# Optimization experiments

Measured on AMD Instinct MI355X. Metric: run time of the kernel, lower is better.

## Reference

```python
import jax, jax.numpy as jnp
import numpy as np

KNN = 5
MAX_STEPS = 100
LAM = 1.0  # bound_lambda


def setup_inputs() -> dict:
    key = jax.random.key(0)
    k1, k2 = jax.random.split(key)
    # probabilities in (0,1): softmax-like scores
    scores_raw = jax.random.uniform(k1, (1, 8192, 8, 8), dtype=jnp.float32)
    feats = jax.random.normal(k2, (1, 8192, 256, 1, 1), dtype=jnp.float32)
    return {"scores_raw": scores_raw, "feats": feats}


def knn_affinity(X, knn):
    # X: (N, D) L2-normalized features. Same math as torch.norm(x_i - x_j):
    # ||xi-xj|| = sqrt(|xi|^2 + |xj|^2 - 2 xi.xj), avoids the O(N^2 D) broadcast.
    N = X.shape[0]
    sq = jnp.sum(X * X, axis=-1)                                  # (N,)
    dist2 = sq[:, None] + sq[None, :] - 2.0 * (X @ X.T)           # (N, N)
    dist = jnp.sqrt(jnp.maximum(dist2, 0.0))
    n_neighbors = min(knn + 1, N)
    _, idx = jax.lax.top_k(-dist, n_neighbors)                    # smallest distances
    idx = idx[:, 1:]                                              # drop self
    W = jnp.zeros((N, N), X.dtype).at[jnp.arange(N)[:, None], idx].set(1.0)
    return W


def reference(scores_raw, feats):
    _, _, H, W = scores_raw.shape
    unary = -jnp.log(scores_raw.reshape(-1, H * W) + 1e-10)       # (N, K)
    f = feats.reshape(feats.shape[0], feats.shape[1], -1)[0]       # (N, D), flatten(-3).squeeze(0)
    nrm = jnp.linalg.norm(f, axis=-1, keepdims=True)
    f = f / jnp.maximum(nrm, 1e-12)                                # F.normalize(p=2)
    kernel = knn_affinity(f, KNN)                                  # (N, N)

    Y0 = jax.nn.softmax(-unary, axis=-1)

    def cond(state):
        i, Y, oldE, conv = state
        return (i < MAX_STEPS) & (~conv)

    def body(state):
        i, Y, oldE, _ = state
        pairwise = LAM * (kernel @ Y)                              # (N, K)
        Ynew = jax.nn.softmax(-unary + pairwise, axis=-1)
        # entropy_energy (note: lambda multiplies pairwise again, as in source)
        E = jnp.sum(unary * Ynew - LAM * pairwise * Ynew
                    + Ynew * jnp.log(jnp.clip(Ynew, 1e-20)))
        conv = (i > 1) & (jnp.abs(E - oldE) <= 1e-8 * jnp.abs(oldE))
        return (i + 1, Ynew, E, conv)

    init = (jnp.int32(0), Y0, jnp.float32(jnp.inf), jnp.bool_(False))
    _, Y, _, _ = jax.lax.while_loop(cond, body, init)
    return Y
```

## Files before the change

kernel.cpp:

```cpp
#include <hip/hip_runtime.h>
#include <math.h>

#define NROWS 8192
#define DIM   256
#define NCLS  64
#define KNN   5
#define NCAND 8
#define NSPLIT 4
#define MAXSTEPS 100
#define PBLK 256

struct GS {
  double Eold;
  double Epart[PBLK];
  int pad0[30];
  int gcnt[16 * 32];
  int root; int pad1[31];
  int gen;  int pad2[31];
  int flag; int pad3[31];
};

typedef __attribute__((ext_vector_type(8))) short bf16x8;
typedef __attribute__((ext_vector_type(4))) float f32x4;

typedef __attribute__((address_space(1))) unsigned int glb_u32_t;
typedef __attribute__((address_space(3))) unsigned int lds_u32_t;
__device__ __forceinline__ void async_cp16(const uint4* g, uint4* l) {
  __builtin_amdgcn_global_load_lds((const glb_u32_t*)(const unsigned int*)g,
                                   (lds_u32_t*)(unsigned int*)l, 16, 0, 0);
}

__device__ __forceinline__ float aloadf(const float* p) {
  return __hip_atomic_load(p, __ATOMIC_RELAXED, __HIP_MEMORY_SCOPE_AGENT);
}
__device__ __forceinline__ void astoref(float* p, float v) {
  __hip_atomic_store(p, v, __ATOMIC_RELAXED, __HIP_MEMORY_SCOPE_AGENT);
}
__device__ __forceinline__ double aloadd(const double* p) {
  return __hip_atomic_load(p, __ATOMIC_RELAXED, __HIP_MEMORY_SCOPE_AGENT);
}
__device__ __forceinline__ void astored(double* p, double v) {
  __hip_atomic_store(p, v, __ATOMIC_RELAXED, __HIP_MEMORY_SCOPE_AGENT);
}
__device__ __forceinline__ int aloadi(const int* p) {
  return __hip_atomic_load(p, __ATOMIC_RELAXED, __HIP_MEMORY_SCOPE_AGENT);
}
__device__ __forceinline__ void astorei(int* p, int v) {
  __hip_atomic_store(p, v, __ATOMIC_RELAXED, __HIP_MEMORY_SCOPE_AGENT);
}
__device__ __forceinline__ int afetchadd(int* p) {
  return __hip_atomic_fetch_add(p, 1, __ATOMIC_RELAXED, __HIP_MEMORY_SCOPE_AGENT);
}

__device__ __forceinline__ float wave_sum64(float v) {
#pragma unroll
  for (int m = 32; m >= 1; m >>= 1) v += __shfl_xor(v, m, 64);
  return v;
}
__device__ __forceinline__ double wave_sum64d(double v) {
#pragma unroll
  for (int m = 32; m >= 1; m >>= 1) v += __shfl_xor(v, m, 64);
  return v;
}

__device__ __forceinline__ unsigned short f2bf(float x) {
  unsigned u = __float_as_uint(x);
  u += 0x7FFFu + ((u >> 16) & 1u);
  return (unsigned short)(u >> 16);
}

__global__ void k_normalize(const float* __restrict__ feats, uint2* __restrict__ fb2,
                            float* __restrict__ f, double* __restrict__ sqd) {
  int row  = blockIdx.x * 4 + (threadIdx.x >> 6);
  int lane = threadIdx.x & 63;
  float4 v = ((const float4*)(feats + (size_t)row * DIM))[lane];
  double ss = (double)v.x * v.x + (double)v.y * v.y + (double)v.z * v.z + (double)v.w * v.w;
  ss = wave_sum64d(ss);
  float nr = fmaxf((float)sqrt(ss), 1e-12f);
  float4 o;
  o.x = v.x / nr; o.y = v.y / nr; o.z = v.z / nr; o.w = v.w / nr;
  ((float4*)(f + (size_t)row * DIM))[lane] = o;
  double s2 = (double)o.x * o.x + (double)o.y * o.y + (double)o.z * o.z + (double)o.w * o.w;
  s2 = wave_sum64d(s2);
  if (lane == 0) sqd[row] = s2;
  uint2 w2;
  w2.x = (unsigned)f2bf(o.x) | ((unsigned)f2bf(o.y) << 16);
  w2.y = (unsigned)f2bf(o.z) | ((unsigned)f2bf(o.w) << 16);
  int T = row >> 6, rl = row & 63, g = lane >> 1, h = lane & 1;
  fb2[((size_t)T * 2048 + rl * 32 + (g ^ (rl & 31))) * 2 + h] = w2;
}

#define JSPAN (NROWS / NSPLIT)
#define GTILES (JSPAN / 64)

__launch_bounds__(256, 2)
__global__ void k_gram(const uint4* __restrict__ fb, int* __restrict__ candp) {
  __shared__ uint4 Bsh4[2][2048];
  __shared__ float Csh[4096];

  const int t  = threadIdx.x;
  const int ib = blockIdx.x >> 2;
  const int js = blockIdx.x & 3;
  const int i0 = ib * 64;
  const int jbase = js * JSPAN;
  const int w = t >> 6, lane = t & 63;

  {
    const uint4* At = fb + (size_t)ib * 2048;
    const uint4* Bt = fb + (size_t)(js * 32) * 2048;
#pragma unroll
    for (int p = 0; p < 8; ++p) {
      int c = w * 8 + p;
      async_cp16(At + c * 64 + lane, &Bsh4[1][c * 64]);
      async_cp16(Bt + c * 64 + lane, &Bsh4[0][c * 64]);
    }
  }
  const int ihalf = w >> 1, jhalf = w & 1;
  const int m15 = lane & 15, quad = lane >> 4;

  __syncthreads();

  bf16x8 areg[2][8];
#pragma unroll
  for (int s = 0; s < 2; ++s) {
    int ra = ihalf * 32 + s * 16 + m15;
#pragma unroll
    for (int kc = 0; kc < 8; ++kc)
      areg[s][kc] = ((const bf16x8*)Bsh4[1])[ra * 32 + ((kc * 4 + quad) ^ (ra & 31))];
  }
  __syncthreads();

  unsigned mk[NCAND];
#pragma unroll
  for (int k = 0; k < NCAND; ++k) mk[k] = 0u;
  float thr = -1e30f;

  const int trow = lane >> 1;
  const int thalf = lane & 1;
  float* Csw = Csh + w * 1024;

  for (int jt = 0; jt < GTILES; ++jt) {
    const int cbuf = jt & 1;
    if (jt > 0) __syncthreads();
    if (jt + 1 < GTILES) {
      const uint4* Bt = fb + (size_t)(js * 32 + jt + 1) * 2048;
#pragma unroll
      for (int p = 0; p < 8; ++p) {
        int c = w * 8 + p;
        async_cp16(Bt + c * 64 + lane, &Bsh4[1 - cbuf][c * 64]);
      }
    }

    f32x4 acc[2][2];
#pragma unroll
    for (int si = 0; si < 2; ++si)
#pragma unroll
      for (int sj = 0; sj < 2; ++sj) acc[si][sj] = (f32x4)(0.f);

#pragma unroll
    for (int kc = 0; kc < 8; ++kc) {
      bf16x8 bv[2];
#pragma unroll
      for (int s = 0; s < 2; ++s) {
        int rb = jhalf * 32 + s * 16 + m15;
        bv[s] = ((const bf16x8*)Bsh4[cbuf])[rb * 32 + ((kc * 4 + quad) ^ (rb & 31))];
      }
      acc[0][0] = __builtin_amdgcn_mfma_f32_16x16x32_bf16(areg[0][kc], bv[0], acc[0][0], 0, 0, 0);
      acc[0][1] = __builtin_amdgcn_mfma_f32_16x16x32_bf16(areg[0][kc], bv[1], acc[0][1], 0, 0, 0);
      acc[1][0] = __builtin_amdgcn_mfma_f32_16x16x32_bf16(areg[1][kc], bv[0], acc[1][0], 0, 0, 0);
      acc[1][1] = __builtin_amdgcn_mfma_f32_16x16x32_bf16(areg[1][kc], bv[1], acc[1][1], 0, 0, 0);
    }

#pragma unroll
    for (int si = 0; si < 2; ++si)
#pragma unroll
      for (int sj = 0; sj < 2; ++sj) {
        int lr0 = si * 16 + quad * 4;
        int key = quad * 2;
        int lc = sj * 16 + m15;
        int gc = lc >> 2;
        int base = lr0 * 32 + ((gc ^ key) << 2) + (lc & 3);
#pragma unroll
        for (int r = 0; r < 4; ++r)
          Csw[base + r * 32] = acc[si][sj][r];
      }

    {
      int cb0 = jt * 64 + jhalf * 32;
      int skey = (trow >> 1) & 6;
#pragma unroll
      for (int p = 0; p < 4; ++p) {
        int gc = thalf * 4 + p;
        float4 v = *(const float4*)&Csw[trow * 32 + ((gc ^ skey) << 2)];
        float g4 = fmaxf(fmaxf(v.x, v.y), fmaxf(v.z, v.w));
        if (g4 > thr) {
          int cbase = cb0 + gc * 4;
          float vv[4] = {v.x, v.y, v.z, v.w};
#pragma unroll
          for (int e = 0; e < 4; ++e) {
            unsigned ub = __float_as_uint(vv[e]);
            unsigned key = ((ub ^ (unsigned)(((int)ub >> 31) | 0x80000000)) & ~2047u)
                           | (unsigned)(cbase + e);
            if (key > mk[NCAND - 1]) {
              mk[NCAND - 1] = key;
#pragma unroll
              for (int q = NCAND - 1; q >= 1; --q)
                if (mk[q] > mk[q - 1]) { unsigned tm = mk[q]; mk[q] = mk[q - 1]; mk[q - 1] = tm; }
            }
          }
          unsigned kb = mk[NCAND - 1] & ~2047u;
          if (kb) {
            unsigned xm = 0x80000000u | ~(unsigned)((int)kb >> 31);
            thr = __uint_as_float(kb ^ xm);
          }
        }
      }
    }
  }

  __syncthreads();
  unsigned* mergeK = (unsigned*)Csh;
  {
    int grow = ihalf * 32 + trow;
    int q = jhalf * 2 + thalf;
#pragma unroll
    for (int k = 0; k < NCAND; ++k) mergeK[grow * 33 + q * 8 + k] = mk[k];
  }
  __syncthreads();
  if (t < 64) {
    unsigned fk[NCAND];
#pragma unroll
    for (int k = 0; k < NCAND; ++k) fk[k] = 0u;
    for (int s = 0; s < 32; ++s) {
      unsigned kk = mergeK[t * 33 + s];
      if (kk > fk[NCAND - 1]) {
        fk[NCAND - 1] = kk;
#pragma unroll
        for (int q = NCAND - 1; q >= 1; --q)
          if (fk[q] > fk[q - 1]) { unsigned tm = fk[q]; fk[q] = fk[q - 1]; fk[q - 1] = tm; }
      }
    }
#pragma unroll
    for (int k = 0; k < NCAND; ++k)
      candp[(size_t)js * (NROWS * NCAND) + (size_t)(i0 + t) * NCAND + k] =
          jbase + (int)(fk[k] & 2047u);
  }
}

__global__ void k_refine(const float* __restrict__ f, const double* __restrict__ sqd,
                         const int* __restrict__ candp, int* __restrict__ nbr) {
  const int row = blockIdx.x * 4 + (threadIdx.x >> 6);
  const int t = threadIdx.x & 63;
  const int c = t >> 1;
  const int seg = t & 1;
  const int split = c >> 3, slot = c & 7;
  int j = candp[(size_t)split * (NROWS * NCAND) + (size_t)row * NCAND + slot];
  const float4* fi4 = (const float4*)(f + (size_t)row * DIM) + seg * 32;
  const float4* fj4 = (const float4*)(f + (size_t)j * DIM) + seg * 32;
  double dot = 0.0;
#pragma unroll 8
  for (int d4 = 0; d4 < 32; ++d4) {
    float4 a = fi4[d4], b = fj4[d4];
    dot = fma((double)a.x, (double)b.x, dot);
    dot = fma((double)a.y, (double)b.y, dot);
    dot = fma((double)a.z, (double)b.z, dot);
    dot = fma((double)a.w, (double)b.w, dot);
  }
  dot += __shfl_xor(dot, 1, 64);
  double key = sqd[j] - 2.0 * dot;
  bool valid = (seg == 0) && (j != row);
  for (int s = 0; s < KNN; ++s) {
    double v = valid ? key : (double)INFINITY;
    int vj = valid ? j : 0x7fffffff;
#pragma unroll
    for (int m = 1; m < 64; m <<= 1) {
      double ov = __shfl_xor(v, m, 64);
      int oj = __shfl_xor(vj, m, 64);
      if (ov < v || (ov == v && oj < vj)) { v = ov; vj = oj; }
    }
    if (valid && vj == j) valid = false;
    if (t == 0) nbr[(size_t)row * 8 + s] = vj;
  }
}

__global__ void k_solve(const float* __restrict__ scores,
                        const int* __restrict__ nbr,
                        float* __restrict__ Ya, float* __restrict__ Yb,
                        float* __restrict__ out, GS* __restrict__ gs) {
  const int b = blockIdx.x;
  const int w = threadIdx.x >> 6, lane = threadIdx.x & 63;
  const int row0 = b * 32 + w * 4;
  const int grp = (b & 15) * 32;
  __shared__ int nbl[32][5];
  __shared__ double sE[8];
  __shared__ int sflag;

  if (threadIdx.x < 160)
    nbl[threadIdx.x / 5][threadIdx.x % 5] =
        nbr[(size_t)(b * 32 + threadIdx.x / 5) * 8 + (threadIdx.x % 5)];

  float u[4], y[4];
#pragma unroll
  for (int r = 0; r < 4; ++r)
    u[r] = -logf(scores[(size_t)(row0 + r) * NCLS + lane] + 1e-10f);
#pragma unroll
  for (int r = 0; r < 4; ++r) {
    float e = expf(-u[r]);
    float sum = wave_sum64(e);
    y[r] = e / sum;
    astoref(&Ya[(size_t)(row0 + r) * NCLS + lane], y[r]);
  }
  __syncthreads();

  int nboff[4][KNN];
#pragma unroll
  for (int r = 0; r < 4; ++r)
#pragma unroll
    for (int k = 0; k < KNN; ++k)
      nboff[r][k] = nbl[w * 4 + r][k] * NCLS + lane;

  int mygen = 1;
  if (threadIdx.x == 0) {
    __builtin_amdgcn_fence(__ATOMIC_RELEASE, "workgroup");
    int old = afetchadd(&gs->gcnt[grp]);
    if (old == 15) {
      int r = afetchadd(&gs->root);
      if (r == 15) {
#pragma unroll
        for (int m = 0; m < 16; ++m) astorei(&gs->gcnt[m * 32], 0);
        astorei(&gs->root, 0);
        __builtin_amdgcn_fence(__ATOMIC_RELEASE, "workgroup");
        astorei(&gs->gen, mygen);
      }
    }
    while (aloadi(&gs->gen) < mygen) __builtin_amdgcn_s_sleep(1);
  }
  __syncthreads();
  ++mygen;

  for (int iter = 0; iter < MAXSTEPS; ++iter) {
    const float* __restrict__ Yin = (iter & 1) ? Yb : Ya;
    float* __restrict__ Yout = (iter & 1) ? Ya : Yb;
    double ew = 0.0;
#pragma unroll
    for (int r = 0; r < 4; ++r) {
      float pw = 0.f;
#pragma unroll
      for (int k = 0; k < KNN; ++k) pw += aloadf(&Yin[nboff[r][k]]);
      float e = expf(pw - u[r]);
      float sum = wave_sum64(e);
      y[r] = e / sum;
      astoref(&Yout[(size_t)(row0 + r) * NCLS + lane], y[r]);
      ew += -(double)logf(sum);
    }
    if (lane == 0) sE[w] = ew;
    __syncthreads();
    if (w == 0) {
      double be = (lane < 8) ? sE[lane] : 0.0;
      be = wave_sum64d(be);
      int last = 0;
      if (lane == 0) {
        astored(&gs->Epart[b], be);
        __builtin_amdgcn_fence(__ATOMIC_RELEASE, "workgroup");
        int old = afetchadd(&gs->gcnt[grp]);
        if (old == 15) {
          int r = afetchadd(&gs->root);
          last = (r == 15);
        }
      }
      last = __shfl(last, 0, 64);
      if (last) {
        double s = 0.0;
#pragma unroll
        for (int i = 0; i < 4; ++i) s += aloadd(&gs->Epart[lane + 64 * i]);
        s = wave_sum64d(s);
        if (lane < 16) astorei(&gs->gcnt[lane * 32], 0);
        if (lane == 0) {
          astorei(&gs->root, 0);
          double eo = aloadd(&gs->Eold);
          int conv = (iter > 1) && (fabs(s - eo) <= 1e-8 * fabs(eo));
          astorei(&gs->flag, conv);
          if (!conv) astored(&gs->Eold, s);
        }
        __builtin_amdgcn_fence(__ATOMIC_RELEASE, "workgroup");
        if (lane == 0) astorei(&gs->gen, mygen);
      }
      if (lane == 0) {
        while (aloadi(&gs->gen) < mygen) __builtin_amdgcn_s_sleep(1);
        sflag = aloadi(&gs->flag);
      }
    }
    __syncthreads();
    ++mygen;
    if (sflag) break;
  }

#pragma unroll
  for (int r = 0; r < 4; ++r)
    out[(size_t)(row0 + r) * NCLS + lane] = y[r];
}

__global__ void k_init(GS* gs) {
  int t = threadIdx.x;
  if (t == 0) {
    gs->Eold = (double)INFINITY;
    gs->root = 0; gs->gen = 0; gs->flag = 0;
  }
  if (t < 16 * 32) gs->gcnt[t] = 0;
}

extern "C" void kernel_launch(void* const* d_in, const int* in_sizes, int n_in,
                              void* d_out, int out_size, void* d_ws, size_t ws_size,
                              hipStream_t stream) {
  (void)in_sizes; (void)n_in; (void)out_size; (void)ws_size;
  const float* scores = (const float*)d_in[0];
  const float* feats  = (const float*)d_in[1];
  float* out = (float*)d_out;
  char* ws = (char*)d_ws;
  uint4*  fb    = (uint4*)(ws + 0);
  float*  f     = (float*)(ws + 4194304);
  float*  Ya    = (float*)(ws + 4194304);
  float*  Yb    = (float*)(ws + 6291456);
  double* sqd   = (double*)(ws + 12582912);
  int*    candp = (int*)(ws + 12648448);
  int*    nbr   = (int*)(ws + 13697024);
  GS*     gs    = (GS*)(ws + 13959168);

  k_init<<<1, 512, 0, stream>>>(gs);
  k_normalize<<<NROWS / 4, 256, 0, stream>>>(feats, (uint2*)fb, f, sqd);
  k_gram<<<(NROWS / 64) * NSPLIT, 256, 0, stream>>>(fb, candp);
  k_refine<<<NROWS / 4, 256, 0, stream>>>(f, sqd, candp, nbr);
  k_solve<<<PBLK, 512, 0, stream>>>(scores, nbr, Ya, Yb, out, gs);
}
```

Baseline: 262.8 us.

## Run top-k selection directly on MFMA accumulators instead of staging through LDS

The MFMA operands are swapped so each lane's accumulator registers hold four consecutive columns of one row. Each lane then keeps per-row candidate lists in registers and filters them straight from the accumulators, which removes the per-tile LDS write and read of the Gram tile. The final merge now combines 64 partial lists per row instead of 32, using a rotated LDS layout. In exchange, each lane keeps two candidate lists and thresholds, which raises register pressure, and the serial merge done by one wave becomes longer.

Result: faster. 246.1 us (-6.3%).

```diff
diff --git a/kernel.cpp b/kernel.cpp
--- a/kernel.cpp
+++ b/kernel.cpp
@@ -96,7 +96,7 @@
 __launch_bounds__(256, 2)
 __global__ void k_gram(const uint4* __restrict__ fb, int* __restrict__ candp) {
   __shared__ uint4 Bsh4[2][2048];
-  __shared__ float Csh[4096];
+  __shared__ unsigned Ksh[4096];
 
   const int t  = threadIdx.x;
   const int ib = blockIdx.x >> 2;
@@ -115,7 +115,7 @@
       async_cp16(Bt + c * 64 + lane, &Bsh4[0][c * 64]);
     }
   }
-  const int ihalf = w >> 1, jhalf = w & 1;
+  const int ahalf = w >> 1, bhalf = w & 1;
   const int m15 = lane & 15, quad = lane >> 4;
 
   __syncthreads();
@@ -123,21 +123,19 @@
   bf16x8 areg[2][8];
 #pragma unroll
   for (int s = 0; s < 2; ++s) {
-    int ra = ihalf * 32 + s * 16 + m15;
+    int ra = ahalf * 32 + s * 16 + m15;
 #pragma unroll
     for (int kc = 0; kc < 8; ++kc)
       areg[s][kc] = ((const bf16x8*)Bsh4[1])[ra * 32 + ((kc * 4 + quad) ^ (ra & 31))];
   }
   __syncthreads();
 
-  unsigned mk[NCAND];
-#pragma unroll
-  for (int k = 0; k < NCAND; ++k) mk[k] = 0u;
-  float thr = -1e30f;
-
-  const int trow = lane >> 1;
-  const int thalf = lane & 1;
-  float* Csw = Csh + w * 1024;
+  unsigned mk[2][NCAND];
+#pragma unroll
+  for (int s = 0; s < 2; ++s)
+#pragma unroll
+    for (int k = 0; k < NCAND; ++k) mk[s][k] = 0u;
+  float thr[2] = {-1e30f, -1e30f};
 
   for (int jt = 0; jt < GTILES; ++jt) {
     const int cbuf = jt & 1;
@@ -155,84 +153,73 @@
 #pragma unroll
     for (int si = 0; si < 2; ++si)
 #pragma unroll
-      for (int sj = 0; sj < 2; ++sj) acc[si][sj] = (f32x4)(0.f);
+      for (int s = 0; s < 2; ++s) acc[si][s] = (f32x4)(0.f);
 
 #pragma unroll
     for (int kc = 0; kc < 8; ++kc) {
       bf16x8 bv[2];
 #pragma unroll
+      for (int si = 0; si < 2; ++si) {
+        int rb = bhalf * 32 + si * 16 + m15;
+        bv[si] = ((const bf16x8*)Bsh4[cbuf])[rb * 32 + ((kc * 4 + quad) ^ (rb & 31))];
+      }
+      acc[0][0] = __builtin_amdgcn_mfma_f32_16x16x32_bf16(bv[0], areg[0][kc], acc[0][0], 0, 0, 0);
+      acc[0][1] = __builtin_amdgcn_mfma_f32_16x16x32_bf16(bv[0], areg[1][kc], acc[0][1], 0, 0, 0);
+      acc[1][0] = __builtin_amdgcn_mfma_f32_16x16x32_bf16(bv[1], areg[0][kc], acc[1][0], 0, 0, 0);
+      acc[1][1] = __builtin_amdgcn_mfma_f32_16x16x32_bf16(bv[1], areg[1][kc], acc[1][1], 0, 0, 0);
+    }
+
+    {
+      const unsigned cbase = (unsigned)(jt * 64 + bhalf * 32 + quad * 4);
+#pragma unroll
       for (int s = 0; s < 2; ++s) {
-        int rb = jhalf * 32 + s * 16 + m15;
-        bv[s] = ((const bf16x8*)Bsh4[cbuf])[rb * 32 + ((kc * 4 + quad) ^ (rb & 31))];
-      }
-      acc[0][0] = __builtin_amdgcn_mfma_f32_16x16x32_bf16(areg[0][kc], bv[0], acc[0][0], 0, 0, 0);
-      acc[0][1] = __builtin_amdgcn_mfma_f32_16x16x32_bf16(areg[0][kc], bv[1], acc[0][1], 0, 0, 0);
-      acc[1][0] = __builtin_amdgcn_mfma_f32_16x16x32_bf16(areg[1][kc], bv[0], acc[1][0], 0, 0, 0);
-      acc[1][1] = __builtin_amdgcn_mfma_f32_16x16x32_bf16(areg[1][kc], bv[1], acc[1][1], 0, 0, 0);
-    }
-
-#pragma unroll
-    for (int si = 0; si < 2; ++si)
-#pragma unroll
-      for (int sj = 0; sj < 2; ++sj) {
-        int lr0 = si * 16 + quad * 4;
-        int key = quad * 2;
-        int lc = sj * 16 + m15;
-        int gc = lc >> 2;
-        int base = lr0 * 32 + ((gc ^ key) << 2) + (lc & 3);
-#pragma unroll
-        for (int r = 0; r < 4; ++r)
-          Csw[base + r * 32] = acc[si][sj][r];
-      }
-
-    {
-      int cb0 = jt * 64 + jhalf * 32;
-      int skey = (trow >> 1) & 6;
-#pragma unroll
-      for (int p = 0; p < 4; ++p) {
-        int gc = thalf * 4 + p;
-        float4 v = *(const float4*)&Csw[trow * 32 + ((gc ^ skey) << 2)];
-        float g4 = fmaxf(fmaxf(v.x, v.y), fmaxf(v.z, v.w));
-        if (g4 > thr) {
-          int cbase = cb0 + gc * 4;
-          float vv[4] = {v.x, v.y, v.z, v.w};
-#pragma unroll
-          for (int e = 0; e < 4; ++e) {
-            unsigned ub = __float_as_uint(vv[e]);
-            unsigned key = ((ub ^ (unsigned)(((int)ub >> 31) | 0x80000000)) & ~2047u)
-                           | (unsigned)(cbase + e);
-            if (key > mk[NCAND - 1]) {
-              mk[NCAND - 1] = key;
-#pragma unroll
-              for (int q = NCAND - 1; q >= 1; --q)
-                if (mk[q] > mk[q - 1]) { unsigned tm = mk[q]; mk[q] = mk[q - 1]; mk[q - 1] = tm; }
+#pragma unroll
+        for (int si = 0; si < 2; ++si) {
+          f32x4 v = acc[si][s];
+          float g4 = fmaxf(fmaxf(v[0], v[1]), fmaxf(v[2], v[3]));
+          if (g4 > thr[s]) {
+            unsigned cb = cbase + (unsigned)(si * 16);
+#pragma unroll
+            for (int e = 0; e < 4; ++e) {
+              unsigned ub = __float_as_uint(v[e]);
+              unsigned key = ((ub ^ (unsigned)(((int)ub >> 31) | 0x80000000)) & ~2047u)
+                             | (cb + (unsigned)e);
+              if (key > mk[s][NCAND - 1]) {
+                mk[s][NCAND - 1] = key;
+#pragma unroll
+                for (int q = NCAND - 1; q >= 1; --q)
+                  if (mk[s][q] > mk[s][q - 1]) {
+                    unsigned tm = mk[s][q]; mk[s][q] = mk[s][q - 1]; mk[s][q - 1] = tm;
+                  }
+              }
             }
           }
-          unsigned kb = mk[NCAND - 1] & ~2047u;
-          if (kb) {
-            unsigned xm = 0x80000000u | ~(unsigned)((int)kb >> 31);
-            thr = __uint_as_float(kb ^ xm);
-          }
         }
-      }
-    }
-  }
-
-  __syncthreads();
-  unsigned* mergeK = (unsigned*)Csh;
-  {
-    int grow = ihalf * 32 + trow;
-    int q = jhalf * 2 + thalf;
-#pragma unroll
-    for (int k = 0; k < NCAND; ++k) mergeK[grow * 33 + q * 8 + k] = mk[k];
+        unsigned kb = mk[s][NCAND - 1] & ~2047u;
+        if (kb) {
+          unsigned xm = 0x80000000u | ~(unsigned)((int)kb >> 31);
+          thr[s] = __uint_as_float(kb ^ xm);
+        }
+      }
+    }
+  }
+
+  __syncthreads();
+#pragma unroll
+  for (int s = 0; s < 2; ++s) {
+    int row = ahalf * 32 + s * 16 + m15;
+    int slot0 = bhalf * 32 + quad * 8;
+#pragma unroll
+    for (int k = 0; k < NCAND; ++k)
+      Ksh[row * 64 + ((slot0 + k + row) & 63)] = mk[s][k];
   }
   __syncthreads();
   if (t < 64) {
     unsigned fk[NCAND];
 #pragma unroll
     for (int k = 0; k < NCAND; ++k) fk[k] = 0u;
-    for (int s = 0; s < 32; ++s) {
-      unsigned kk = mergeK[t * 33 + s];
+    for (int s = 0; s < 64; ++s) {
+      unsigned kk = Ksh[t * 64 + ((s + t) & 63)];
       if (kk > fk[NCAND - 1]) {
         fk[NCAND - 1] = kk;
 #pragma unroll
```
